# Kernel tuning notes

Hardware: AMD Instinct MI355X
Metric: run time of the kernel (lower is better)

The kernel has to match this reference:

```python
import jax, jax.numpy as jnp
import numpy as np

N_PTS = 65536   # input points
M = 4096        # sampled clusters (n_nodes)
K = 16          # knn neighbors
C_IN = 128
C_OUT = 256
BN_EPS = 1e-5


def setup_inputs() -> dict:
    key = jax.random.key(0)
    k1, k2, k3 = jax.random.split(key, 3)
    x = jax.random.normal(k1, (N_PTS, C_IN), jnp.float32)
    pos = jax.random.normal(k2, (N_PTS, 3), jnp.float32)
    batch = jnp.zeros((N_PTS,), jnp.int32)  # single point cloud
    W = jax.random.normal(k3, (C_IN, C_OUT), jnp.float32) / np.sqrt(C_IN)
    b = jnp.zeros((C_OUT,), jnp.float32)
    gamma = jnp.ones((C_OUT,), jnp.float32)
    beta = jnp.zeros((C_OUT,), jnp.float32)
    return {"x": x, "pos": pos, "batch": batch, "W": W, "b": b,
            "gamma": gamma, "beta": beta}


def _fps(pos, m):
    """Farthest point sampling starting from index 0. Returns m indices."""
    n = pos.shape[0]

    def step(carry, _):
        min_d, last = carry
        d = jnp.sum((pos - pos[last]) ** 2, axis=-1)  # [N]
        min_d = jnp.minimum(min_d, d)
        nxt = jnp.argmax(min_d).astype(jnp.int32)
        return (min_d, nxt), nxt

    init = (jnp.full((n,), jnp.inf, pos.dtype), jnp.int32(0))
    _, rest = jax.lax.scan(step, init, None, length=m - 1)
    return jnp.concatenate([jnp.zeros((1,), jnp.int32), rest])


def _knn(pos, sub_pos, k):
    """For each of M query points, indices of k nearest points in pos. [M, k]"""
    # squared euclidean distances, [M, N]
    d2 = (jnp.sum(sub_pos ** 2, -1, keepdims=True)
          - 2.0 * sub_pos @ pos.T
          + jnp.sum(pos ** 2, -1)[None, :])
    _, idx = jax.lax.top_k(-d2, k)
    return idx


def _mlp(x, W, b, gamma, beta):
    # Linear -> BatchNorm1d (training-mode batch stats, biased var) -> ReLU
    h = x @ W + b                      # [N, C_OUT]
    mu = jnp.mean(h, axis=0)
    var = jnp.mean((h - mu) ** 2, axis=0)
    h = gamma * (h - mu) * jax.lax.rsqrt(var + BN_EPS) + beta
    return jax.nn.relu(h)


def reference(x, pos, batch, W, b, gamma, beta):
    id_clusters = _fps(pos, M)                 # [M]
    sub_pos = pos[id_clusters]                 # [M, 3]
    sub_batch = batch[id_clusters]             # [M]
    nbr = _knn(pos, sub_pos, K)                # [M, K]
    h = _mlp(x, W, b, gamma, beta)             # [N, C_OUT]
    # gather + max-pool over each cluster's k neighbors (== scatter_max,
    # since knn emits exactly K neighbors per cluster, grouped by cluster)
    out = jnp.max(h[nbr], axis=1)              # [M, C_OUT]
    return out, sub_pos, sub_batch
```

## Files before the change

### kernel.cpp

```cpp
#include <hip/hip_runtime.h>
#include <hip/hip_bf16.h>

#define N_PTS 65536
#define MCLUS 4096
#define KNN   16
#define C_IN  128
#define C_OUT 256

typedef unsigned long long u64;
typedef unsigned u32;
typedef unsigned short u16;

#define WS_ID     0
#define WS_SLOTS  16384
#define WS_SCALE  16384
#define WS_SHIFT  17408
#define WS_BBOX   49152
#define WS_CNT    49216
#define WS_NBR    49216
#define WS_OFS    180288
#define WS_POS4   311360
#define WS_PSUM   311360
#define WS_PSUMSQ 835648

__device__ __forceinline__ u32 fkey(float v) {
    u32 u = __float_as_uint(v);
    return (u >> 31) ? ~u : (u | 0x80000000u);
}
__device__ __forceinline__ float funkey(u32 k) {
    u32 u = (k >> 31) ? (k & 0x7FFFFFFFu) : ~k;
    return __uint_as_float(u);
}

__global__ void init_kernel(int* __restrict__ id, u64* __restrict__ slots,
                            u32* __restrict__ bbox, int* __restrict__ cellcnt) {
    int t = threadIdx.x;
    for (int i = t; i < 4096; i += 1024) slots[i] = 0ull;
    for (int i = t; i < 32768; i += 1024) cellcnt[i] = 0;
    if (t < 3)   bbox[t] = 0xFFFFFFFFu;
    if (t >= 3 && t < 6) bbox[t] = 0u;
    if (t == 0) id[0] = 0;
}

__global__ __launch_bounds__(256) void bbox_kernel(const float* __restrict__ pos,
                                                   u32* __restrict__ bbox) {
    int t = blockIdx.x * 256 + threadIdx.x;
    u32 mn0 = 0xFFFFFFFFu, mn1 = 0xFFFFFFFFu, mn2 = 0xFFFFFFFFu;
    u32 mx0 = 0u, mx1 = 0u, mx2 = 0u;
    for (int i = t; i < N_PTS; i += 16384) {
        u32 k0 = fkey(pos[i*3+0]), k1 = fkey(pos[i*3+1]), k2 = fkey(pos[i*3+2]);
        mn0 = min(mn0, k0); mn1 = min(mn1, k1); mn2 = min(mn2, k2);
        mx0 = max(mx0, k0); mx1 = max(mx1, k1); mx2 = max(mx2, k2);
    }
    #pragma unroll
    for (int off = 32; off > 0; off >>= 1) {
        mn0 = min(mn0, (u32)__shfl_xor(mn0, off)); mx0 = max(mx0, (u32)__shfl_xor(mx0, off));
        mn1 = min(mn1, (u32)__shfl_xor(mn1, off)); mx1 = max(mx1, (u32)__shfl_xor(mx1, off));
        mn2 = min(mn2, (u32)__shfl_xor(mn2, off)); mx2 = max(mx2, (u32)__shfl_xor(mx2, off));
    }
    if ((threadIdx.x & 63) == 0) {
        atomicMin(&bbox[0], mn0); atomicMin(&bbox[1], mn1); atomicMin(&bbox[2], mn2);
        atomicMax(&bbox[3], mx0); atomicMax(&bbox[4], mx1); atomicMax(&bbox[5], mx2);
    }
}

__device__ __forceinline__ int morton32(int gx, int gy, int gz) {
    int m = 0;
    #pragma unroll
    for (int k = 0; k < 5; ++k)
        m |= (((gx >> k) & 1) << (3*k + 2)) | (((gy >> k) & 1) << (3*k + 1)) | (((gz >> k) & 1) << (3*k));
    return m;
}

__device__ __forceinline__ int cell_of(float x, float y, float z, const u32* bb) {
    float x0 = funkey(bb[0]), y0 = funkey(bb[1]), z0 = funkey(bb[2]);
    float x1 = funkey(bb[3]), y1 = funkey(bb[4]), z1 = funkey(bb[5]);
    float sx = 32.0f / fmaxf(x1 - x0, 1e-20f);
    float sy = 32.0f / fmaxf(y1 - y0, 1e-20f);
    float sz = 32.0f / fmaxf(z1 - z0, 1e-20f);
    int gx = min(max((int)((x - x0) * sx), 0), 31);
    int gy = min(max((int)((y - y0) * sy), 0), 31);
    int gz = min(max((int)((z - z0) * sz), 0), 31);
    return morton32(gx, gy, gz);
}

__global__ __launch_bounds__(256) void count_kernel(const float* __restrict__ pos,
                                                    const u32* __restrict__ bbox,
                                                    int* __restrict__ cellcnt) {
    int i = blockIdx.x * 256 + threadIdx.x;
    atomicAdd(&cellcnt[cell_of(pos[i*3+0], pos[i*3+1], pos[i*3+2], bbox)], 1);
}

__global__ __launch_bounds__(1024) void scan_kernel(const int* __restrict__ cellcnt,
                                                    int* __restrict__ cellofs) {
    __shared__ int ts[1024];
    int t = threadIdx.x;
    int v[32]; int s = 0;
    #pragma unroll
    for (int i = 0; i < 32; ++i) { v[i] = cellcnt[t*32 + i]; s += v[i]; }
    ts[t] = s; __syncthreads();
    for (int off = 1; off < 1024; off <<= 1) {
        int u = (t >= off) ? ts[t - off] : 0;
        __syncthreads();
        ts[t] += u;
        __syncthreads();
    }
    int pre = (t == 0) ? 0 : ts[t - 1];
    #pragma unroll
    for (int i = 0; i < 32; ++i) { cellofs[t*32 + i] = pre; pre += v[i]; }
}

__global__ __launch_bounds__(256) void scatter_kernel(const float* __restrict__ pos,
                                                      const u32* __restrict__ bbox,
                                                      int* __restrict__ cellofs,
                                                      float4* __restrict__ pos4) {
    int i = blockIdx.x * 256 + threadIdx.x;
    float x = pos[i*3+0], y = pos[i*3+1], z = pos[i*3+2];
    int o = atomicAdd(&cellofs[cell_of(x, y, z, bbox)], 1);
    pos4[o] = make_float4(x, y, z, __int_as_float(i));
}

__device__ __forceinline__ float dist3(float ax, float ay, float az,
                                       float bx, float by, float bz) {
    float dx = __fsub_rn(ax, bx), dy = __fsub_rn(ay, by), dz = __fsub_rn(az, bz);
    return __fadd_rn(__fadd_rn(__fmul_rn(dx, dx), __fmul_rn(dy, dy)), __fmul_rn(dz, dz));
}

__device__ __forceinline__ u32 wave_max_u32(u32 v) {
    #pragma unroll
    for (int off = 32; off > 0; off >>= 1) {
        u32 o = __shfl_xor(v, off);
        v = o > v ? o : v;
    }
    return v;
}
__device__ __forceinline__ u32 wave_min_u32(u32 v) {
    #pragma unroll
    for (int off = 32; off > 0; off >>= 1) {
        u32 o = __shfl_xor(v, off);
        v = o < v ? o : v;
    }
    return v;
}

__device__ __forceinline__ int wave_argmax48(u64 k48) {
    u32 hi = (u32)(k48 >> 16);
    u32 him = wave_max_u32(hi);
    u64 ball = __ballot(hi == him);
    if (__popcll(ball) > 1) {
        u32 a = (hi == him) ? (u32)(k48 & 0xFFFFull) : 0u;
        u32 am = wave_max_u32(a);
        ball = __ballot((hi == him) && (a == am));
    }
    return __ffsll((long long)ball) - 1;
}

__global__ __launch_bounds__(64) void fps_kernel(const float* __restrict__ pos,
                                                 const float4* __restrict__ pos4,
                                                 int* __restrict__ id,
                                                 u64* __restrict__ slots) {
    const int lane = threadIdx.x;
    const int blk  = blockIdx.x;
    __shared__ float bku[1024];

    float px[16], py[16], pz[16], md[16];
    u32 inv[16];
    const float c0x = pos[0], c0y = pos[1], c0z = pos[2];
    #pragma unroll
    for (int e = 0; e < 16; ++e) {
        int sp = blk * 1024 + (lane >> 3) * 128 + e * 8 + (lane & 7);
        float4 v = pos4[sp];
        px[e] = v.x; py[e] = v.y; pz[e] = v.z;
        inv[e] = 0xFFFFu - (u32)__float_as_int(v.w);
        md[e] = dist3(px[e], py[e], pz[e], c0x, c0y, c0z);
    }

    int r = 0;
    u32 fb_mine = 0xFu;

    auto slow_round = [&](int rr, int s) {
        u64 bk = 0; float bx = 0.f, by = 0.f, bz = 0.f;
        #pragma unroll
        for (int e = 0; e < 16; ++e) {
            u64 k = ((u64)__float_as_uint(md[e]) << 16) | inv[e];
            bool bt = k > bk;
            bk = bt ? k : bk; bx = bt ? px[e] : bx; by = bt ? py[e] : by; bz = bt ? pz[e] : bz;
        }
        int src = wave_argmax48(bk);
        float wx = __shfl(bx, src), wy = __shfl(by, src), wz = __shfl(bz, src);
        u64 kb = __shfl(bk, src);

        const u64 tg = (u64)((rr + 1) & 0xFFFF);
        u64* base = &slots[(u32)(rr & 1) * 2048];
        {
            u64 w0 = (kb << 16) | tg;
            u64 w1 = ((u64)__float_as_uint(wx) << 32) | tg;
            u64 w2 = ((u64)__float_as_uint(wy) << 32) | tg;
            u64 w3 = ((u64)__float_as_uint(wz) << 32) | tg;
            u64 wv = (lane == 0) ? w0 : (lane == 1) ? w1 : (lane == 2) ? w2 : w3;
            if (lane < 4)
                __hip_atomic_store(&base[(u32)blk * 32 + (u32)lane], wv,
                                   __ATOMIC_RELAXED, __HIP_MEMORY_SCOPE_AGENT);
        }
        u64* bp = &base[(u32)lane * 32];
        u64 v0, v1, v2, v3;
        for (;;) {
            v0 = __hip_atomic_load(&bp[0], __ATOMIC_RELAXED, __HIP_MEMORY_SCOPE_AGENT);
            v1 = __hip_atomic_load(&bp[1], __ATOMIC_RELAXED, __HIP_MEMORY_SCOPE_AGENT);
            v2 = __hip_atomic_load(&bp[2], __ATOMIC_RELAXED, __HIP_MEMORY_SCOPE_AGENT);
            v3 = __hip_atomic_load(&bp[3], __ATOMIC_RELAXED, __HIP_MEMORY_SCOPE_AGENT);
            u64 bad = ((v0 ^ tg) | (v1 ^ tg) | (v2 ^ tg) | (v3 ^ tg)) & 0xFFFFull;
            if (bad == 0ull) break;
        }
        u64 k2 = v0 >> 16;
        int s2 = wave_argmax48(k2);
        u64 kw = __shfl(k2, s2);
        float cx = __shfl(__uint_as_float((u32)(v1 >> 32)), s2);
        float cy = __shfl(__uint_as_float((u32)(v2 >> 32)), s2);
        float cz = __shfl(__uint_as_float((u32)(v3 >> 32)), s2);
        if (blk == 0 && lane == 0) id[s] = (int)(0xFFFFu - (u32)(kw & 0xFFFFull));
        #pragma unroll
        for (int e = 0; e < 16; ++e)
            md[e] = fminf(md[e], dist3(px[e], py[e], pz[e], cx, cy, cz));
    };

    u64 wk48[8]; float wxa[8], wya[8], wza[8];

    for (int B = 0; B <= 511; ++B) {
        u64 bk = 0; float bx = 0.f, by = 0.f, bz = 0.f;
        #pragma unroll
        for (int e = 0; e < 16; ++e) {
            u64 k = ((u64)__float_as_uint(md[e]) << 16) | inv[e];
            bool bt = k > bk;
            bk = bt ? k : bk; bx = bt ? px[e] : bx; by = bt ? py[e] : by; bz = bt ? pz[e] : bz;
        }
        u64 ks = bk;
        #pragma unroll
        for (int off = 1; off <= 4; off <<= 1) {
            u64 o = __shfl_xor(ks, off);
            if (o > ks) ks = o;
        }
        {
            u64 ball = __ballot(bk == ks);
            int segbase = (lane >> 3) << 3;
            int ssrc = __ffsll((long long)(ball & (0xFFull << segbase))) - 1;
            bx = __shfl(bx, ssrc); by = __shfl(by, ssrc); bz = __shfl(bz, ssrc);
        }

        const u64 tg = (u64)((r + 1) & 0xFFFF);
        u64* base = &slots[(u32)(r & 1) * 2048];
        {
            int c = lane / 3; if (c > 7) c = 7;
            int p = lane - c * 3;
            int srcl = 8 * c;
            u64 kk  = __shfl(ks, srcl);
            float gx = __shfl(bx, srcl), gy = __shfl(by, srcl), gz = __shfl(bz, srcl);
            u32 hi, mid;
            if (p == 0)      { hi = __float_as_uint(gx); mid = (u32)(kk & 0xFFFFull); }
            else if (p == 1) { hi = __float_as_uint(gy); mid = (u32)(kk >> 32) & 0xFFFFu; }
            else             { hi = __float_as_uint(gz); mid = (u32)(kk >> 16) & 0xFFFFu; }
            u64 wd = ((u64)hi << 32) | ((u64)mid << 16) | tg;
            if (lane == 24) wd = ((u64)(fb_mine & 0xFu) << 16) | tg;
            if (lane < 25)
                __hip_atomic_store(&base[(u32)blk * 32 + (u32)lane], wd,
                                   __ATOMIC_RELAXED, __HIP_MEMORY_SCOPE_AGENT);
        }

        u64 w[25]; u32 valid = 0;
        {
            u64* bp = &base[(u32)lane * 32];
            do {
                #pragma unroll
                for (int i = 0; i < 25; ++i)
                    if (!(valid & (1u << i)))
                        w[i] = __hip_atomic_load(&bp[i], __ATOMIC_RELAXED, __HIP_MEMORY_SCOPE_AGENT);
                #pragma unroll
                for (int i = 0; i < 25; ++i)
                    if ((u32)(w[i] & 0xFFFFull) == (u32)tg) valid |= (1u << i);
            } while (valid != 0x1FFFFFFu);
        }
        ++r;

        u32 jstar = wave_min_u32((u32)(w[24] >> 16) & 0xFu);
        if (jstar < 8u) {
            #pragma unroll
            for (int e = 0; e < 16; ++e) md[e] = bku[e * 64 + lane];
            #pragma unroll
            for (int j = 0; j < 8; ++j) {
                if ((u32)j < jstar) {
                    #pragma unroll
                    for (int e = 0; e < 16; ++e)
                        md[e] = fminf(md[e], dist3(px[e], py[e], pz[e], wxa[j], wya[j], wza[j]));
                }
            }
            int sbase = 8 * (B - 1) + 1;
            for (int sub = (int)jstar; sub < 8; ++sub) { slow_round(r, sbase + sub); ++r; }
            fb_mine = 0xFu;
            --B; continue;
        }
        if (B == 511) break;

        float cpx[8], cpy[8], cpz[8], cmdf[8]; u32 cinv[8];
        #pragma unroll
        for (int c = 0; c < 8; ++c) {
            u64 a = w[3 * c], b = w[3 * c + 1], d = w[3 * c + 2];
            cpx[c] = __uint_as_float((u32)(a >> 32));
            cpy[c] = __uint_as_float((u32)(b >> 32));
            cpz[c] = __uint_as_float((u32)(d >> 32));
            cinv[c] = (u32)(a >> 16) & 0xFFFFu;
            u32 mdb = (((u32)(b >> 16) & 0xFFFFu) << 16) | ((u32)(d >> 16) & 0xFFFFu);
            cmdf[c] = __uint_as_float(mdb);
        }

        float pwx = 0.f, pwy = 0.f, pwz = 0.f;
        #pragma unroll
        for (int j = 0; j < 8; ++j) {
            if (j) {
                #pragma unroll
                for (int c = 0; c < 8; ++c)
                    cmdf[c] = fminf(cmdf[c], dist3(cpx[c], cpy[c], cpz[c], pwx, pwy, pwz));
            }
            u64 bk2 = 0; float b2x = 0.f, b2y = 0.f, b2z = 0.f;
            #pragma unroll
            for (int c = 0; c < 8; ++c) {
                u64 k = ((u64)__float_as_uint(cmdf[c]) << 16) | cinv[c];
                bool bt = k > bk2;
                bk2 = bt ? k : bk2; b2x = bt ? cpx[c] : b2x; b2y = bt ? cpy[c] : b2y; b2z = bt ? cpz[c] : b2z;
            }
            int src = wave_argmax48(bk2);
            u64 kw = __shfl(bk2, src);
            float wx = __shfl(b2x, src), wy = __shfl(b2y, src), wz = __shfl(b2z, src);
            wk48[j] = kw; wxa[j] = wx; wya[j] = wy; wza[j] = wz;
            pwx = wx; pwy = wy; pwz = wz;
            if (blk == 0 && lane == 0) id[8 * B + 1 + j] = (int)(0xFFFFu - (u32)(kw & 0xFFFFull));
        }

        #pragma unroll
        for (int e = 0; e < 16; ++e) bku[e * 64 + lane] = md[e];
        u32 vmask = 0;
        #pragma unroll
        for (int j = 0; j < 8; ++j) {
            #pragma unroll
            for (int e = 0; e < 16; ++e) {
                u64 vk = ((u64)__float_as_uint(md[e]) << 16) | inv[e];
                if (vk > wk48[j]) vmask |= (1u << j);
            }
            #pragma unroll
            for (int e = 0; e < 16; ++e)
                md[e] = fminf(md[e], dist3(px[e], py[e], pz[e], wxa[j], wya[j], wza[j]));
        }
        #pragma unroll
        for (int off = 32; off > 0; off >>= 1) vmask |= (u32)__shfl_xor(vmask, off);
        fb_mine = vmask ? (u32)(__ffs(vmask) - 1) : 0xFu;
    }

    for (int s = 4089; s < 4096; ++s) { slow_round(r, s); ++r; }
}

__global__ void subout_kernel(const float* __restrict__ pos, const int* __restrict__ batch,
                              const int* __restrict__ id, float* __restrict__ sub_pos,
                              int* __restrict__ sub_batch) {
    int m = blockIdx.x * blockDim.x + threadIdx.x;
    if (m >= MCLUS) return;
    int idx = id[m];
    sub_pos[m*3+0] = pos[idx*3+0];
    sub_pos[m*3+1] = pos[idx*3+1];
    sub_pos[m*3+2] = pos[idx*3+2];
    sub_batch[m] = batch[idx];
}

__global__ __launch_bounds__(64) void knn_kernel(const float* __restrict__ pos,
                                                 const float4* __restrict__ pos4,
                                                 const int* __restrict__ cellend,
                                                 const u32* __restrict__ bbox,
                                                 const int* __restrict__ id,
                                                 u16* __restrict__ nbr) {
    const int q = blockIdx.x;
    const int lane = threadIdx.x;
    const int qi = id[q];
    const float qx = pos[qi*3+0], qy = pos[qi*3+1], qz = pos[qi*3+2];
    const float nq = __fadd_rn(__fadd_rn(__fmul_rn(qx,qx), __fmul_rn(qy,qy)), __fmul_rn(qz,qz));

    const float x0 = funkey(bbox[0]), y0 = funkey(bbox[1]), z0 = funkey(bbox[2]);
    const float x1 = funkey(bbox[3]), y1 = funkey(bbox[4]), z1 = funkey(bbox[5]);
    const float sx = 32.0f / fmaxf(x1 - x0, 1e-20f);
    const float sy = 32.0f / fmaxf(y1 - y0, 1e-20f);
    const float sz = 32.0f / fmaxf(z1 - z0, 1e-20f);
    const float wx = (x1 - x0) * 0.03125f, wy = (y1 - y0) * 0.03125f, wz = (z1 - z0) * 0.03125f;
    const float wmin = fminf(wx, fminf(wy, wz));
    const int gx = min(max((int)((qx - x0) * sx), 0), 31);
    const int gy = min(max((int)((qy - y0) * sy), 0), 31);
    const int gz = min(max((int)((qz - z0) * sz), 0), 31);

    float dl[KNN]; int il[KNN];
    #pragma unroll
    for (int t = 0; t < KNN; ++t) { dl[t] = __builtin_inff(); il[t] = 0x7FFFFFFF; }

    __shared__ float sd[64][KNN];
    __shared__ int   si[64][KNN];

    auto merge16 = [&](bool writeOut) -> float {
        #pragma unroll
        for (int t = 0; t < KNN; ++t) { sd[lane][t] = dl[t]; si[lane][t] = il[t]; }
        __syncthreads();
        int ptr = 0; u64 m = 0;
        for (int rr = 0; rr < KNN; ++rr) {
            u64 key = ~0ull;
            if (ptr < KNN) {
                u32 u = __float_as_uint(sd[lane][ptr]);
                u32 mu = (u >> 31) ? ~u : (u | 0x80000000u);
                key = ((u64)mu << 32) | (u32)si[lane][ptr];
            }
            m = key;
            #pragma unroll
            for (int off = 32; off > 0; off >>= 1) {
                u64 o = __shfl_xor(m, off);
                if (o < m) m = o;
            }
            if (key == m) ptr++;
            if (writeOut && lane == 0) nbr[q*KNN + rr] = (u16)(m & 0xFFFFull);
        }
        __syncthreads();
        return funkey((u32)(m >> 32));
    };

    float B = __builtin_inff();
    for (int R = 0; R < 32; ++R) {
        const int D = 2*R + 1;
        const int F = D*D;
        const int S = (R == 0) ? 1 : (24*R*R + 2);
        bool any = false;
        for (int bas = 0; bas < S; bas += 64) {
            int i = bas + lane;
            int start = 0, len = 0;
            if (i < S) {
                int dx, dy, dz;
                if (R == 0) { dx = 0; dy = 0; dz = 0; }
                else if (i < 2*F) {
                    dz = (i < F) ? -R : R;
                    int k = (i < F) ? i : i - F;
                    dx = k % D - R; dy = k / D - R;
                } else {
                    int j = i - 2*F, P = 8*R;
                    dz = -R + 1 + j / P;
                    int k = j % P;
                    if (k < D)            { dx = k - R;          dy = -R; }
                    else if (k < 2*D)     { dx = (k - D) - R;    dy =  R; }
                    else {
                        int k3 = k - 2*D;
                        if (k3 < 2*R - 1) { dx = -R; dy = k3 - R + 1; }
                        else              { dx =  R; dy = (k3 - (2*R - 1)) - R + 1; }
                    }
                }
                int cx = gx + dx, cy = gy + dy, cz = gz + dz;
                if ((u32)cx < 32u && (u32)cy < 32u && (u32)cz < 32u) {
                    float lx = (cx == 0)  ? -3.4e38f : x0 + (float)cx * wx;
                    float hx = (cx == 31) ?  3.4e38f : x0 + (float)(cx+1) * wx;
                    float ly = (cy == 0)  ? -3.4e38f : y0 + (float)cy * wy;
                    float hy = (cy == 31) ?  3.4e38f : y0 + (float)(cy+1) * wy;
                    float lz = (cz == 0)  ? -3.4e38f : z0 + (float)cz * wz;
                    float hz = (cz == 31) ?  3.4e38f : z0 + (float)(cz+1) * wz;
                    float ddx = fmaxf(fmaxf(lx - qx, qx - hx), 0.f);
                    float ddy = fmaxf(fmaxf(ly - qy, qy - hy), 0.f);
                    float ddz = fmaxf(fmaxf(lz - qz, qz - hz), 0.f);
                    float md2 = ddx*ddx + ddy*ddy + ddz*ddz;
                    if (md2 * 0.999f - 1e-3f <= B) {
                        int mc = morton32(cx, cy, cz);
                        int end = cellend[mc];
                        start = mc ? cellend[mc-1] : 0;
                        len = end - start;
                    }
                }
            }
            u32 pre = (u32)len;
            #pragma unroll
            for (int off = 1; off < 64; off <<= 1) {
                u32 o = __shfl_up(pre, off);
                if (lane >= off) pre += o;
            }
            u32 T = __shfl(pre, 63);
            pre -= (u32)len;
            if (T == 0) continue;
            any = true;
            u32 Tpad = (T + 63u) & ~63u;
            for (u32 t = (u32)lane; t < Tpad; t += 64) {
                bool act = (t < T);
                u32 tt = act ? t : (T - 1u);
                int s = 0;
                #pragma unroll
                for (int step = 32; step > 0; step >>= 1) {
                    int c = s + step;
                    u32 pc = (u32)__shfl(pre, c);
                    if (pc <= tt) s = c;
                }
                u32 p0 = (u32)__shfl(pre, s);
                int st = __shfl(start, s);
                float4 pt = pos4[st + (int)(tt - p0)];
                float npj = __fadd_rn(__fadd_rn(__fmul_rn(pt.x,pt.x), __fmul_rn(pt.y,pt.y)), __fmul_rn(pt.z,pt.z));
                float dot = __fadd_rn(__fadd_rn(__fmul_rn(qx,pt.x), __fmul_rn(qy,pt.y)), __fmul_rn(qz,pt.z));
                float d2  = __fadd_rn(__fsub_rn(nq, __fmul_rn(2.0f, dot)), npj);
                int oi = __float_as_int(pt.w);
                if (act && (d2 < dl[KNN-1] || (d2 == dl[KNN-1] && oi < il[KNN-1]))) {
                    dl[KNN-1] = d2; il[KNN-1] = oi;
                    #pragma unroll
                    for (int t2 = KNN-1; t2 > 0; --t2) {
                        float a = dl[t2-1], bq = dl[t2];
                        int   ai = il[t2-1], bi = il[t2];
                        bool sw = (bq < a) || (bq == a && bi < ai);
                        dl[t2-1] = sw ? bq : a;  dl[t2] = sw ? a : bq;
                        il[t2-1] = sw ? bi : ai; il[t2] = sw ? ai : bi;
                    }
                }
            }
        }
        if (any) B = merge16(false);
        float rw = (float)R * wmin;
        if (rw * rw * 0.999f - 1e-3f > B) break;
    }
    merge16(true);
}

__global__ __launch_bounds__(256) void stats_kernel(const float* __restrict__ x,
                                                    const float* __restrict__ W,
                                                    const float* __restrict__ b,
                                                    float* __restrict__ psum,
                                                    float* __restrict__ psumsq) {
    __shared__ float xl[64*128];
    const int tid = threadIdx.x;
    const int cg = (tid & 63) * 4;
    const int rq = tid >> 6;
    float s0=0,s1=0,s2v=0,s3=0, q0=0,q1=0,q2=0,q3=0;
    const float4 bv = *(const float4*)&b[cg];

    for (int t = 0; t < 2; ++t) {
        const size_t row0 = (size_t)blockIdx.x*128 + (size_t)t*64;
        __syncthreads();
        for (int i = tid*4; i < 64*128; i += 1024)
            *(float4*)&xl[i] = *(const float4*)&x[row0*128 + i];
        __syncthreads();

        float acc[16][4];
        #pragma unroll
        for (int rr = 0; rr < 16; ++rr) { acc[rr][0]=bv.x; acc[rr][1]=bv.y; acc[rr][2]=bv.z; acc[rr][3]=bv.w; }

        for (int k4 = 0; k4 < 32; ++k4) {
            float4 w0 = *(const float4*)&W[(k4*4+0)*256 + cg];
            float4 w1 = *(const float4*)&W[(k4*4+1)*256 + cg];
            float4 w2 = *(const float4*)&W[(k4*4+2)*256 + cg];
            float4 w3 = *(const float4*)&W[(k4*4+3)*256 + cg];
            #pragma unroll
            for (int rr = 0; rr < 16; ++rr) {
                float4 xv = *(float4*)&xl[(rq*16+rr)*128 + k4*4];
                acc[rr][0] = fmaf(xv.w,w3.x, fmaf(xv.z,w2.x, fmaf(xv.y,w1.x, fmaf(xv.x,w0.x, acc[rr][0]))));
                acc[rr][1] = fmaf(xv.w,w3.y, fmaf(xv.z,w2.y, fmaf(xv.y,w1.y, fmaf(xv.x,w0.y, acc[rr][1]))));
                acc[rr][2] = fmaf(xv.w,w3.z, fmaf(xv.z,w2.z, fmaf(xv.y,w1.z, fmaf(xv.x,w0.z, acc[rr][2]))));
                acc[rr][3] = fmaf(xv.w,w3.w, fmaf(xv.z,w2.w, fmaf(xv.y,w1.w, fmaf(xv.x,w0.w, acc[rr][3]))));
            }
        }
        #pragma unroll
        for (int rr = 0; rr < 16; ++rr) {
            s0 += acc[rr][0]; q0 = fmaf(acc[rr][0],acc[rr][0],q0);
            s1 += acc[rr][1]; q1 = fmaf(acc[rr][1],acc[rr][1],q1);
            s2v+= acc[rr][2]; q2 = fmaf(acc[rr][2],acc[rr][2],q2);
            s3 += acc[rr][3]; q3 = fmaf(acc[rr][3],acc[rr][3],q3);
        }
    }
    __syncthreads();
    float* red = xl;
    red[rq*256 + cg+0] = s0; red[rq*256 + cg+1] = s1; red[rq*256 + cg+2] = s2v; red[rq*256 + cg+3] = s3;
    red[1024 + rq*256 + cg+0] = q0; red[1024 + rq*256 + cg+1] = q1;
    red[1024 + rq*256 + cg+2] = q2; red[1024 + rq*256 + cg+3] = q3;
    __syncthreads();
    if (rq == 0) {
        #pragma unroll
        for (int c = 0; c < 4; ++c) {
            int ch = cg + c;
            float ss = red[ch] + red[256+ch] + red[512+ch] + red[768+ch];
            float qq = red[1024+ch] + red[1280+ch] + red[1536+ch] + red[1792+ch];
            psum  [blockIdx.x*256 + ch] = ss;
            psumsq[blockIdx.x*256 + ch] = qq;
        }
    }
}

__global__ void finalize_kernel(const float* __restrict__ psum, const float* __restrict__ psumsq,
                                const float* __restrict__ gamma, const float* __restrict__ beta,
                                float* __restrict__ scale, float* __restrict__ shift) {
    int c = threadIdx.x;
    float s = 0.f, s2 = 0.f;
    for (int bl = 0; bl < 512; ++bl) { s += psum[bl*256+c]; s2 += psumsq[bl*256+c]; }
    float mu  = s  / 65536.0f;
    float var = s2 / 65536.0f - mu*mu;
    float inv = rsqrtf(var + 1e-5f);
    float sc = gamma[c] * inv;
    scale[c] = sc;
    shift[c] = beta[c] - mu * sc;
}

__global__ __launch_bounds__(256) void out_kernel(const float* __restrict__ x,
                                                  const float* __restrict__ W,
                                                  const float* __restrict__ b,
                                                  const u16* __restrict__ nbr,
                                                  const float* __restrict__ scale,
                                                  const float* __restrict__ shift,
                                                  float* __restrict__ out) {
    __shared__ float xl[16*128];
    __shared__ int nb[16];
    const int tid = threadIdx.x;
    const int m = blockIdx.x;
    if (tid < 16) nb[tid] = (int)nbr[m*16 + tid];
    __syncthreads();
    for (int i = tid; i < 16*128; i += 256) {
        int rr = i >> 7, k = i & 127;
        xl[i] = x[(size_t)nb[rr]*128 + k];
    }
    __syncthreads();

    float acc[16];
    const float bias = b[tid];
    #pragma unroll
    for (int rr = 0; rr < 16; ++rr) acc[rr] = bias;

    for (int k4 = 0; k4 < 32; ++k4) {
        float w0 = W[(k4*4+0)*256 + tid];
        float w1 = W[(k4*4+1)*256 + tid];
        float w2 = W[(k4*4+2)*256 + tid];
        float w3 = W[(k4*4+3)*256 + tid];
        #pragma unroll
        for (int rr = 0; rr < 16; ++rr) {
            float4 xv = *(float4*)&xl[rr*128 + k4*4];
            acc[rr] = fmaf(xv.w,w3, fmaf(xv.z,w2, fmaf(xv.y,w1, fmaf(xv.x,w0, acc[rr]))));
        }
    }
    const float sc = scale[tid], sh = shift[tid];
    float v = acc[0];
    #pragma unroll
    for (int rr = 1; rr < 16; ++rr) v = (sc >= 0.f) ? fmaxf(v, acc[rr]) : fminf(v, acc[rr]);
    out[(size_t)m*256 + tid] = fmaxf(fmaf(sc, v, sh), 0.f);
}

extern "C" void kernel_launch(void* const* d_in, const int* in_sizes, int n_in,
                              void* d_out, int out_size, void* d_ws, size_t ws_size,
                              hipStream_t stream) {
    const float* x     = (const float*)d_in[0];
    const float* pos   = (const float*)d_in[1];
    const int*   batch = (const int*)  d_in[2];
    const float* W     = (const float*)d_in[3];
    const float* b     = (const float*)d_in[4];
    const float* gamma = (const float*)d_in[5];
    const float* beta  = (const float*)d_in[6];

    float* out      = (float*)d_out;
    float* sub_pos  = out + (size_t)MCLUS*C_OUT;
    int*   sub_batch= (int*)(out + (size_t)MCLUS*C_OUT + (size_t)MCLUS*3);

    char* ws = (char*)d_ws;
    int*    id      = (int*)   (ws + WS_ID);
    u64*    slots   = (u64*)   (ws + WS_SLOTS);
    float*  scalep  = (float*) (ws + WS_SCALE);
    float*  shiftp  = (float*) (ws + WS_SHIFT);
    u32*    bbox    = (u32*)   (ws + WS_BBOX);
    int*    cellcnt = (int*)   (ws + WS_CNT);
    u16*    nbr     = (u16*)   (ws + WS_NBR);
    int*    cellofs = (int*)   (ws + WS_OFS);
    float4* pos4    = (float4*)(ws + WS_POS4);
    float*  psum    = (float*) (ws + WS_PSUM);
    float*  psumsq  = (float*) (ws + WS_PSUMSQ);

    init_kernel<<<1, 1024, 0, stream>>>(id, slots, bbox, cellcnt);
    bbox_kernel<<<64, 256, 0, stream>>>(pos, bbox);
    count_kernel<<<256, 256, 0, stream>>>(pos, bbox, cellcnt);
    scan_kernel<<<1, 1024, 0, stream>>>(cellcnt, cellofs);
    scatter_kernel<<<256, 256, 0, stream>>>(pos, bbox, cellofs, pos4);
    fps_kernel<<<64, 64, 0, stream>>>(pos, pos4, id, slots);
    subout_kernel<<<16, 256, 0, stream>>>(pos, batch, id, sub_pos, sub_batch);
    knn_kernel<<<MCLUS, 64, 0, stream>>>(pos, pos4, cellofs, bbox, id, nbr);
    stats_kernel<<<512, 256, 0, stream>>>(x, W, b, psum, psumsq);
    finalize_kernel<<<1, 256, 0, stream>>>(psum, psumsq, gamma, beta, scalep, shiftp);
    out_kernel<<<MCLUS, 256, 0, stream>>>(x, W, b, nbr, scalep, shiftp, out);
}
```

Measured before the change: 6.703 ms.

## Place FPS worker blocks on a single XCD via runtime election

The FPS kernel now launches 512 blocks. Each block reports its hardware XCC id, and block 0 elects 64 blocks that share one XCD to do the work while the rest exit. The aim is to keep the FPS cross-block synchronization traffic inside one XCD's L2 rather than crossing dies. It adds a spin-wait election phase with a timeout fallback, plus risks from relying on co-residency and reusing workspace memory for the election words.

After: 9.003 ms. 34.3% more time.

```diff
diff --git a/kernel.cpp b/kernel.cpp
--- a/kernel.cpp
+++ b/kernel.cpp
@@ -17,6 +17,7 @@
 #define WS_SHIFT  17408
 #define WS_BBOX   49152
 #define WS_CNT    49216
+#define WS_REPDEC 49216
 #define WS_NBR    49216
 #define WS_OFS    180288
 #define WS_POS4   311360
@@ -113,7 +114,10 @@
 __global__ __launch_bounds__(256) void scatter_kernel(const float* __restrict__ pos,
                                                       const u32* __restrict__ bbox,
                                                       int* __restrict__ cellofs,
-                                                      float4* __restrict__ pos4) {
+                                                      float4* __restrict__ pos4,
+                                                      u32* __restrict__ repdec) {
+    if (blockIdx.x == 0)
+        for (int i = threadIdx.x; i < 1024; i += 256) repdec[i] = 0u;
     int i = blockIdx.x * 256 + threadIdx.x;
     float x = pos[i*3+0], y = pos[i*3+1], z = pos[i*3+2];
     int o = atomicAdd(&cellofs[cell_of(x, y, z, bbox)], 1);
@@ -158,9 +162,65 @@
 __global__ __launch_bounds__(64) void fps_kernel(const float* __restrict__ pos,
                                                  const float4* __restrict__ pos4,
                                                  int* __restrict__ id,
-                                                 u64* __restrict__ slots) {
+                                                 u64* __restrict__ slots,
+                                                 u32* __restrict__ repdec) {
     const int lane = threadIdx.x;
-    const int blk  = blockIdx.x;
+    const int obk  = blockIdx.x;
+    u32* rep = repdec;
+    u32* dec = repdec + 512;
+
+    u32 xcc;
+    asm volatile("s_getreg_b32 %0, hwreg(20, 0, 4)" : "=s"(xcc));
+    if (lane == 0)
+        __hip_atomic_store(&rep[obk], 0x100u | (xcc & 0xFu),
+                           __ATOMIC_RELAXED, __HIP_MEMORY_SCOPE_AGENT);
+
+    if (obk == 0) {
+        __shared__ u32 srep[512];
+        u64 t0 = __builtin_amdgcn_s_memrealtime();
+        for (;;) {
+            int got = 0;
+            u32 rv[8];
+            #pragma unroll
+            for (int i = 0; i < 8; ++i) {
+                rv[i] = __hip_atomic_load(&rep[lane + 64*i], __ATOMIC_RELAXED, __HIP_MEMORY_SCOPE_AGENT);
+                if (rv[i] & 0x100u) got++;
+            }
+            int tot = got;
+            #pragma unroll
+            for (int off = 32; off > 0; off >>= 1) tot += __shfl_xor(tot, off);
+            u64 t1 = __builtin_amdgcn_s_memrealtime();
+            if (tot >= 512 || (tot >= 64 && (t1 - t0) > 500000ull)) {
+                #pragma unroll
+                for (int i = 0; i < 8; ++i) srep[lane + 64*i] = rv[i];
+                break;
+            }
+        }
+        __syncthreads();
+        if (lane == 0) {
+            int cnt[8] = {0,0,0,0,0,0,0,0};
+            for (int i = 0; i < 512; ++i) if (srep[i] & 0x100u) cnt[srep[i] & 7u]++;
+            int best = 0;
+            for (int x = 1; x < 8; ++x) if (cnt[x] > cnt[best]) best = x;
+            bool byXcd = (cnt[best] >= 64);
+            int p = 0;
+            for (int i = 0; i < 512; ++i) {
+                u32 rv = srep[i];
+                bool ok = (rv & 0x100u) && (p < 64) && (!byXcd || ((rv & 7u) == (u32)best));
+                u32 d = 0x80000000u | (ok ? (u32)p : 0xFFFFu);
+                if (ok) p++;
+                __hip_atomic_store(&dec[i], d, __ATOMIC_RELAXED, __HIP_MEMORY_SCOPE_AGENT);
+            }
+        }
+    }
+
+    u32 myd;
+    do {
+        myd = __hip_atomic_load(&dec[obk], __ATOMIC_RELAXED, __HIP_MEMORY_SCOPE_AGENT);
+    } while (!(myd & 0x80000000u));
+    if ((myd & 0xFFFFu) == 0xFFFFu) return;
+    const int blk = (int)(myd & 0xFFFFu);
+
     __shared__ float bku[1024];
 
     float px[16], py[16], pz[16], md[16];
@@ -661,6 +721,7 @@
     float*  shiftp  = (float*) (ws + WS_SHIFT);
     u32*    bbox    = (u32*)   (ws + WS_BBOX);
     int*    cellcnt = (int*)   (ws + WS_CNT);
+    u32*    repdec  = (u32*)   (ws + WS_REPDEC);
     u16*    nbr     = (u16*)   (ws + WS_NBR);
     int*    cellofs = (int*)   (ws + WS_OFS);
     float4* pos4    = (float4*)(ws + WS_POS4);
@@ -671,8 +732,8 @@
     bbox_kernel<<<64, 256, 0, stream>>>(pos, bbox);
     count_kernel<<<256, 256, 0, stream>>>(pos, bbox, cellcnt);
     scan_kernel<<<1, 1024, 0, stream>>>(cellcnt, cellofs);
-    scatter_kernel<<<256, 256, 0, stream>>>(pos, bbox, cellofs, pos4);
-    fps_kernel<<<64, 64, 0, stream>>>(pos, pos4, id, slots);
+    scatter_kernel<<<256, 256, 0, stream>>>(pos, bbox, cellofs, pos4, repdec);
+    fps_kernel<<<512, 64, 0, stream>>>(pos, pos4, id, slots, repdec);
     subout_kernel<<<16, 256, 0, stream>>>(pos, batch, id, sub_pos, sub_batch);
     knn_kernel<<<MCLUS, 64, 0, stream>>>(pos, pos4, cellofs, bbox, id, nbr);
     stats_kernel<<<512, 256, 0, stream>>>(x, W, b, psum, psumsq);
```
